# Kernel optimization log

Hardware: AMD Instinct MI355X
Metric: run time of the kernel (lower is better)

## Reference

```python
import jax, jax.numpy as jnp
import numpy as np

I, H, O = 64, 128, 1
H2, H4 = H // 2, H // 4


def _lstm(x, Wih, Whh, bih, bhh, collect_outputs=True):
    # x: [B, T, in]; Wih: [4H, in]; Whh: [4H, H]; gate order i, f, g, o (PyTorch).
    Hh = Whh.shape[1]
    B = x.shape[0]
    # Precompute input contribution for all timesteps: [T, B, 4H]
    xg = (jnp.einsum('bti,gi->btg', x, Wih) + bih + bhh).transpose(1, 0, 2)

    def step(carry, xg_t):
        h, c = carry
        g = xg_t + h @ Whh.T
        i, f, gg, o = jnp.split(g, 4, axis=-1)
        i = jax.nn.sigmoid(i)
        f = jax.nn.sigmoid(f)
        gg = jnp.tanh(gg)
        o = jax.nn.sigmoid(o)
        c = f * c + i * gg
        h = o * jnp.tanh(c)
        return (h, c), (h if collect_outputs else None)

    h0 = jnp.zeros((B, Hh), x.dtype)
    c0 = jnp.zeros((B, Hh), x.dtype)
    (hT, cT), hs = jax.lax.scan(step, (h0, c0), xg)
    if collect_outputs:
        return hs.transpose(1, 0, 2), hT  # [B, T, H], [B, H]
    return None, hT


def setup_inputs() -> dict:
    key = jax.random.key(0)
    ks = jax.random.split(key, 13)
    s1 = 1.0 / np.sqrt(H)
    s2 = 1.0 / np.sqrt(H2)
    s3 = 1.0 / np.sqrt(H4)
    u = lambda k, shape, s: jax.random.uniform(k, shape, jnp.float32, -s, s)
    return {
        'x': jax.random.normal(ks[0], (256, 1024, I), jnp.float32),
        'Wih1': u(ks[1], (4 * H, I), s1),
        'Whh1': u(ks[2], (4 * H, H), s1),
        'bih1': u(ks[3], (4 * H,), s1),
        'bhh1': u(ks[4], (4 * H,), s1),
        'Wih2': u(ks[5], (4 * H2, H), s2),
        'Whh2': u(ks[6], (4 * H2, H2), s2),
        'bih2': u(ks[7], (4 * H2,), s2),
        'bhh2': u(ks[8], (4 * H2,), s2),
        'W1': u(ks[9], (H4, H2), s2),
        'b1': u(ks[10], (H4,), s2),
        'W2': u(ks[11], (O, H4), s3),
        'b2': u(ks[12], (O,), s3),
    }


def reference(x, Wih1, Whh1, bih1, bhh1, Wih2, Whh2, bih2, bhh2, W1, b1, W2, b2):
    out1, _ = _lstm(x, Wih1, Whh1, bih1, bhh1, collect_outputs=True)
    # out[:, -1, :] of layer 2 == its final hidden state
    _, hT = _lstm(out1, Wih2, Whh2, bih2, bhh2, collect_outputs=False)
    h = jax.nn.sigmoid(hT @ W1.T + b1)
    return jax.nn.sigmoid(h @ W2.T + b2)
```

## Files before the change

### kernel.cpp

```cpp
#include <hip/hip_runtime.h>
#include <hip/hip_fp16.h>

#define NB   256
#define TT   1024
#define II   64
#define NT   768

typedef _Float16 f16;
typedef _Float16 f16x4 __attribute__((ext_vector_type(4)));
typedef _Float16 hf8 __attribute__((ext_vector_type(8)));
typedef float    ff4 __attribute__((ext_vector_type(4)));

__device__ __forceinline__ float rcp_fast(float x){
    float r; asm("v_rcp_f32 %0, %1" : "=v"(r) : "v"(x)); return r;
}
__device__ __forceinline__ float exp2_fast(float x){
    float r; asm("v_exp_f32 %0, %1" : "=v"(r) : "v"(x)); return r;
}
__device__ __forceinline__ float sigm(float x){
    return rcp_fast(1.0f + exp2_fast(x * -1.44269504f));
}
__device__ __forceinline__ float tanh_f(float x){
    return fmaf(-2.0f, rcp_fast(1.0f + exp2_fast(x * 2.88539008f)), 1.0f);
}


__launch_bounds__(NT, 3)
__global__ void lstm_mfma(const float* __restrict__ x,
                          const float* __restrict__ Wih1, const float* __restrict__ Whh1,
                          const float* __restrict__ bih1, const float* __restrict__ bhh1,
                          const float* __restrict__ Wih2, const float* __restrict__ Whh2,
                          const float* __restrict__ bih2, const float* __restrict__ bhh2,
                          const float* __restrict__ W1,   const float* __restrict__ b1,
                          const float* __restrict__ W2,   const float* __restrict__ b2,
                          float* __restrict__ out)
{
    __shared__ __align__(16) f16 xchunk[64][II];
    __shared__ __align__(16) f16 h1buf[2][128];
    __shared__ __align__(16) f16 h2buf[2][64];
    __shared__ float headbuf[32];

    const int j    = threadIdx.x;
    const int b    = blockIdx.x;
    const int wave = j >> 6;
    const int lane = j & 63;
    const int rho  = lane & 15;
    const int kg   = lane >> 4;
    const bool l2w = (wave >= 8);

    hf8 A[4][6];
    ff4 bias[4];
    #pragma unroll
    for (int i = 0; i < 4; ++i){
        const int tau = 4*wave + i;
        #pragma unroll
        for (int kt = 0; kt < 6; ++kt){
            const int k = 32*kt + kg*8;
            const float* src;
            if (!l2w){
                const int R = (rho & 3)*128 + 4*tau + (rho >> 2);
                src = (k < 64) ? (Wih1 + R*64 + k) : (Whh1 + R*128 + (k - 64));
            } else {
                const int R = (rho & 3)*64 + 4*(tau - 32) + (rho >> 2);
                src = (k < 128) ? (Wih2 + R*128 + k) : (Whh2 + R*64 + (k - 128));
            }
            float4 v0 = *(const float4*)src;
            float4 v1 = *(const float4*)(src + 4);
            hf8 a;
            a[0]=(f16)v0.x; a[1]=(f16)v0.y; a[2]=(f16)v0.z; a[3]=(f16)v0.w;
            a[4]=(f16)v1.x; a[5]=(f16)v1.y; a[6]=(f16)v1.z; a[7]=(f16)v1.w;
            A[i][kt] = a;
        }
        if (!l2w){
            #pragma unroll
            for (int r = 0; r < 4; ++r){
                const int R = r*128 + 4*tau + kg;
                bias[i][r] = bih1[R] + bhh1[R];
            }
        } else {
            #pragma unroll
            for (int r = 0; r < 4; ++r){
                const int R = r*64 + 4*(tau - 32) + kg;
                bias[i][r] = bih2[R] + bhh2[R];
            }
        }
    }

    const int  sel    = rho >> 2;
    const int  myU    = 4*(4*wave + sel - (l2w ? 32 : 0)) + kg;
    const bool writer = ((lane & 3) == 0);
    float c = 0.0f;

    const float* xb = x + (size_t)b * TT * II;

    if (j < 512){
        float4 v = ((const float4*)xb)[j];
        f16x4 w; w[0]=(f16)v.x; w[1]=(f16)v.y; w[2]=(f16)v.z; w[3]=(f16)v.w;
        *(f16x4*)&xchunk[j >> 4][(j & 15)*4] = w;
    } else if (j < 640){
        h1buf[0][j - 512] = (f16)0.0f;
    } else if (j < 704){
        h2buf[0][j - 640] = (f16)0.0f;
    }
    __syncthreads();

    int cur = 0;
    for (int t = 0; t < TT; ++t){
        const bool do_stage = ((t & 31) == 0) && (t + 32 < TT) && (j < 512);
        float4 sv;
        if (do_stage)
            sv = ((const float4*)(xb + (size_t)(t + 32)*II))[j];

        const f16* xr  = xchunk[t & 63];
        const f16* h1c = h1buf[cur];
        const f16* h2c = h2buf[cur];

        ff4 a0 = bias[0], a1 = bias[1], a2 = bias[2], a3 = bias[3];
        #pragma unroll
        for (int kt = 0; kt < 6; ++kt){
            const f16* bp;
            if (!l2w) bp = (kt < 2) ? (xr  + 32*kt       + kg*8)
                                    : (h1c + 32*(kt - 2) + kg*8);
            else      bp = (kt < 4) ? (h1c + 32*kt       + kg*8)
                                    : (h2c + 32*(kt - 4) + kg*8);
            hf8 bf = *(const hf8*)bp;
            a0 = __builtin_amdgcn_mfma_f32_16x16x32_f16(A[0][kt], bf, a0, 0, 0, 0);
            a1 = __builtin_amdgcn_mfma_f32_16x16x32_f16(A[1][kt], bf, a1, 0, 0, 0);
            a2 = __builtin_amdgcn_mfma_f32_16x16x32_f16(A[2][kt], bf, a2, 0, 0, 0);
            a3 = __builtin_amdgcn_mfma_f32_16x16x32_f16(A[3][kt], bf, a3, 0, 0, 0);
        }

        ff4 a = (sel >= 2) ? ((sel & 1) ? a3 : a2) : ((sel & 1) ? a1 : a0);
        float hv;
        if (l2w && t == 0){
            hv = 0.0f;
        } else {
            float ig = sigm(a[0]);
            float fg = sigm(a[1]);
            float gg = tanh_f(a[2]);
            float og = sigm(a[3]);
            c  = fg*c + ig*gg;
            hv = og * tanh_f(c);
        }
        if (writer){
            if (l2w) h2buf[cur ^ 1][myU] = (f16)hv;
            else     h1buf[cur ^ 1][myU] = (f16)hv;
        }

        if (do_stage){
            f16x4 w; w[0]=(f16)sv.x; w[1]=(f16)sv.y; w[2]=(f16)sv.z; w[3]=(f16)sv.w;
            *(f16x4*)&xchunk[((t + 32) & 63) + (j >> 4)][(j & 15)*4] = w;
        }
        __syncthreads();
        cur ^= 1;
    }

    if (l2w){
        const f16* h1c = h1buf[0];
        const f16* h2c = h2buf[0];
        ff4 a0 = bias[0], a1 = bias[1], a2 = bias[2], a3 = bias[3];
        #pragma unroll
        for (int kt = 0; kt < 6; ++kt){
            const f16* bp = (kt < 4) ? (h1c + 32*kt + kg*8)
                                     : (h2c + 32*(kt - 4) + kg*8);
            hf8 bf = *(const hf8*)bp;
            a0 = __builtin_amdgcn_mfma_f32_16x16x32_f16(A[0][kt], bf, a0, 0, 0, 0);
            a1 = __builtin_amdgcn_mfma_f32_16x16x32_f16(A[1][kt], bf, a1, 0, 0, 0);
            a2 = __builtin_amdgcn_mfma_f32_16x16x32_f16(A[2][kt], bf, a2, 0, 0, 0);
            a3 = __builtin_amdgcn_mfma_f32_16x16x32_f16(A[3][kt], bf, a3, 0, 0, 0);
        }
        ff4 a = (sel >= 2) ? ((sel & 1) ? a3 : a2) : ((sel & 1) ? a1 : a0);
        float ig = sigm(a[0]);
        float fg = sigm(a[1]);
        float gg = tanh_f(a[2]);
        float og = sigm(a[3]);
        c = fg*c + ig*gg;
        float hv = og * tanh_f(c);
        if (writer) h2buf[1][myU] = (f16)hv;
    }
    __syncthreads();

    if (j < 32){
        float a = b1[j];
        const float* w = W1 + j*64;
        #pragma unroll
        for (int k = 0; k < 64; ++k) a = fmaf(w[k], (float)h2buf[1][k], a);
        headbuf[j] = sigm(a);
    }
    __syncthreads();
    if (j == 0){
        float a = b2[0];
        #pragma unroll
        for (int k = 0; k < 32; ++k) a = fmaf(W2[k], headbuf[k], a);
        out[b] = sigm(a);
    }
}

extern "C" void kernel_launch(void* const* d_in, const int* in_sizes, int n_in,
                              void* d_out, int out_size, void* d_ws, size_t ws_size,
                              hipStream_t stream)
{
    (void)in_sizes; (void)n_in; (void)d_ws; (void)ws_size; (void)out_size;
    lstm_mfma<<<NB, NT, 0, stream>>>(
        (const float*)d_in[0],
        (const float*)d_in[1], (const float*)d_in[2],
        (const float*)d_in[3], (const float*)d_in[4],
        (const float*)d_in[5], (const float*)d_in[6],
        (const float*)d_in[7], (const float*)d_in[8],
        (const float*)d_in[9], (const float*)d_in[10],
        (const float*)d_in[11], (const float*)d_in[12],
        (float*)d_out);
}
```

Baseline: 1.014 ms.

## Shrink block to 4 waves, each owning 12 gate tiles of both layers

Reduces the block from 12 waves to 4 waves. Each wave now holds weights for 12 MFMA tiles, so one wave can cover rows from both layer 1 and layer 2, and the final gate tile is picked with a select tree. The aim is to make the per-timestep __syncthreads cheaper and to cut cross-wave barrier cost in this latency-bound recurrence. In exchange, each wave runs three times as many serial MFMAs per step, and register pressure rises sharply with 72 hf8 weight fragments plus 12 accumulators.

```diff
diff --git a/kernel.cpp b/kernel.cpp
--- a/kernel.cpp
+++ b/kernel.cpp
@@ -4,7 +4,7 @@
 #define NB   256
 #define TT   1024
 #define II   64
-#define NT   768
+#define NT   256
 
 typedef _Float16 f16;
 typedef _Float16 f16x4 __attribute__((ext_vector_type(4)));
@@ -25,7 +25,7 @@
 }
 
 
-__launch_bounds__(NT, 3)
+__launch_bounds__(NT, 1)
 __global__ void lstm_mfma(const float* __restrict__ x,
                           const float* __restrict__ Wih1, const float* __restrict__ Whh1,
                           const float* __restrict__ bih1, const float* __restrict__ bhh1,
@@ -46,18 +46,18 @@
     const int lane = j & 63;
     const int rho  = lane & 15;
     const int kg   = lane >> 4;
-    const bool l2w = (wave >= 8);
-
-    hf8 A[4][6];
-    ff4 bias[4];
+
+    hf8 A[12][6];
+    ff4 bias[12];
     #pragma unroll
-    for (int i = 0; i < 4; ++i){
-        const int tau = 4*wave + i;
+    for (int i = 0; i < 12; ++i){
+        const int  tau = 12*wave + i;
+        const bool l2  = (tau >= 32);
         #pragma unroll
         for (int kt = 0; kt < 6; ++kt){
             const int k = 32*kt + kg*8;
             const float* src;
-            if (!l2w){
+            if (!l2){
                 const int R = (rho & 3)*128 + 4*tau + (rho >> 2);
                 src = (k < 64) ? (Wih1 + R*64 + k) : (Whh1 + R*128 + (k - 64));
             } else {
@@ -71,112 +71,183 @@
             a[4]=(f16)v1.x; a[5]=(f16)v1.y; a[6]=(f16)v1.z; a[7]=(f16)v1.w;
             A[i][kt] = a;
         }
-        if (!l2w){
-            #pragma unroll
-            for (int r = 0; r < 4; ++r){
-                const int R = r*128 + 4*tau + kg;
-                bias[i][r] = bih1[R] + bhh1[R];
-            }
-        } else {
-            #pragma unroll
-            for (int r = 0; r < 4; ++r){
-                const int R = r*64 + 4*(tau - 32) + kg;
-                bias[i][r] = bih2[R] + bhh2[R];
-            }
-        }
-    }
-
-    const int  sel    = rho >> 2;
-    const int  myU    = 4*(4*wave + sel - (l2w ? 32 : 0)) + kg;
-    const bool writer = ((lane & 3) == 0);
+        #pragma unroll
+        for (int r = 0; r < 4; ++r){
+            if (!l2){ const int R = r*128 + 4*tau + kg;        bias[i][r] = bih1[R] + bhh1[R]; }
+            else    { const int R = r*64  + 4*(tau - 32) + kg; bias[i][r] = bih2[R] + bhh2[R]; }
+        }
+    }
+
+    const int  myTau = 12*wave + rho;
+    const bool isl2  = (myTau >= 32);
+    const int  myU   = isl2 ? 4*(myTau - 32) + kg : 4*myTau + kg;
     float c = 0.0f;
 
     const float* xb = x + (size_t)b * TT * II;
 
-    if (j < 512){
-        float4 v = ((const float4*)xb)[j];
-        f16x4 w; w[0]=(f16)v.x; w[1]=(f16)v.y; w[2]=(f16)v.z; w[3]=(f16)v.w;
-        *(f16x4*)&xchunk[j >> 4][(j & 15)*4] = w;
-    } else if (j < 640){
-        h1buf[0][j - 512] = (f16)0.0f;
-    } else if (j < 704){
-        h2buf[0][j - 640] = (f16)0.0f;
+    {
+        const float4* sp = (const float4*)xb;
+        float4 v0 = sp[2*j], v1 = sp[2*j + 1];
+        hf8 w;
+        w[0]=(f16)v0.x; w[1]=(f16)v0.y; w[2]=(f16)v0.z; w[3]=(f16)v0.w;
+        w[4]=(f16)v1.x; w[5]=(f16)v1.y; w[6]=(f16)v1.z; w[7]=(f16)v1.w;
+        *(hf8*)&xchunk[j >> 3][(j & 7)*8] = w;
+        if (j < 128) h1buf[0][j] = (f16)0.0f;
+        if (j < 64)  h2buf[0][j] = (f16)0.0f;
     }
     __syncthreads();
 
     int cur = 0;
     for (int t = 0; t < TT; ++t){
-        const bool do_stage = ((t & 31) == 0) && (t + 32 < TT) && (j < 512);
-        float4 sv;
-        if (do_stage)
-            sv = ((const float4*)(xb + (size_t)(t + 32)*II))[j];
+        const bool stage = ((t & 31) == 0) && (t + 32 < TT);
+        float4 sv0, sv1;
+        if (stage){
+            const float4* sp = (const float4*)(xb + (size_t)(t + 32)*II);
+            sv0 = sp[2*j]; sv1 = sp[2*j + 1];
+        }
 
         const f16* xr  = xchunk[t & 63];
         const f16* h1c = h1buf[cur];
         const f16* h2c = h2buf[cur];
 
-        ff4 a0 = bias[0], a1 = bias[1], a2 = bias[2], a3 = bias[3];
-        #pragma unroll
-        for (int kt = 0; kt < 6; ++kt){
-            const f16* bp;
-            if (!l2w) bp = (kt < 2) ? (xr  + 32*kt       + kg*8)
-                                    : (h1c + 32*(kt - 2) + kg*8);
-            else      bp = (kt < 4) ? (h1c + 32*kt       + kg*8)
-                                    : (h2c + 32*(kt - 4) + kg*8);
-            hf8 bf = *(const hf8*)bp;
-            a0 = __builtin_amdgcn_mfma_f32_16x16x32_f16(A[0][kt], bf, a0, 0, 0, 0);
-            a1 = __builtin_amdgcn_mfma_f32_16x16x32_f16(A[1][kt], bf, a1, 0, 0, 0);
-            a2 = __builtin_amdgcn_mfma_f32_16x16x32_f16(A[2][kt], bf, a2, 0, 0, 0);
-            a3 = __builtin_amdgcn_mfma_f32_16x16x32_f16(A[3][kt], bf, a3, 0, 0, 0);
-        }
-
-        ff4 a = (sel >= 2) ? ((sel & 1) ? a3 : a2) : ((sel & 1) ? a1 : a0);
+        hf8 bf[8];
+        if (wave <= 2){
+            bf[0] = *(const hf8*)(xr + kg*8);
+            bf[1] = *(const hf8*)(xr + 32 + kg*8);
+        }
+        bf[2] = *(const hf8*)(h1c       + kg*8);
+        bf[3] = *(const hf8*)(h1c + 32  + kg*8);
+        bf[4] = *(const hf8*)(h1c + 64  + kg*8);
+        bf[5] = *(const hf8*)(h1c + 96  + kg*8);
+        if (wave >= 2){
+            bf[6] = *(const hf8*)(h2c      + kg*8);
+            bf[7] = *(const hf8*)(h2c + 32 + kg*8);
+        }
+
+        ff4 acc[12];
+        #pragma unroll
+        for (int i = 0; i < 12; ++i) acc[i] = bias[i];
+
+        if (wave < 2){
+            #pragma unroll
+            for (int kt = 0; kt < 6; ++kt){
+                hf8 bb = bf[kt];
+                #pragma unroll
+                for (int i = 0; i < 12; ++i)
+                    acc[i] = __builtin_amdgcn_mfma_f32_16x16x32_f16(A[i][kt], bb, acc[i], 0, 0, 0);
+            }
+        } else if (wave == 2){
+            #pragma unroll
+            for (int kt = 0; kt < 6; ++kt){
+                hf8 b1f = bf[kt];
+                #pragma unroll
+                for (int i = 0; i < 8; ++i)
+                    acc[i] = __builtin_amdgcn_mfma_f32_16x16x32_f16(A[i][kt], b1f, acc[i], 0, 0, 0);
+                hf8 b2f = bf[kt + 2];
+                #pragma unroll
+                for (int i = 8; i < 12; ++i)
+                    acc[i] = __builtin_amdgcn_mfma_f32_16x16x32_f16(A[i][kt], b2f, acc[i], 0, 0, 0);
+            }
+        } else {
+            #pragma unroll
+            for (int kt = 0; kt < 6; ++kt){
+                hf8 bb = bf[kt + 2];
+                #pragma unroll
+                for (int i = 0; i < 12; ++i)
+                    acc[i] = __builtin_amdgcn_mfma_f32_16x16x32_f16(A[i][kt], bb, acc[i], 0, 0, 0);
+            }
+        }
+
+        ff4 m0 = (rho & 1) ? acc[1]  : acc[0];
+        ff4 m1 = (rho & 1) ? acc[3]  : acc[2];
+        ff4 m2 = (rho & 1) ? acc[5]  : acc[4];
+        ff4 m3 = (rho & 1) ? acc[7]  : acc[6];
+        ff4 m4 = (rho & 1) ? acc[9]  : acc[8];
+        ff4 m5 = (rho & 1) ? acc[11] : acc[10];
+        ff4 n0 = (rho & 2) ? m1 : m0;
+        ff4 n1 = (rho & 2) ? m3 : m2;
+        ff4 n2 = (rho & 2) ? m5 : m4;
+        ff4 p  = (rho & 4) ? n1 : n0;
+        ff4 qd = (rho & 8) ? n2 : p;
+
         float hv;
-        if (l2w && t == 0){
+        if (isl2 && t == 0){
             hv = 0.0f;
         } else {
-            float ig = sigm(a[0]);
-            float fg = sigm(a[1]);
-            float gg = tanh_f(a[2]);
-            float og = sigm(a[3]);
+            float ig = sigm(qd[0]);
+            float fg = sigm(qd[1]);
+            float gg = tanh_f(qd[2]);
+            float og = sigm(qd[3]);
             c  = fg*c + ig*gg;
             hv = og * tanh_f(c);
         }
-        if (writer){
-            if (l2w) h2buf[cur ^ 1][myU] = (f16)hv;
-            else     h1buf[cur ^ 1][myU] = (f16)hv;
-        }
-
-        if (do_stage){
-            f16x4 w; w[0]=(f16)sv.x; w[1]=(f16)sv.y; w[2]=(f16)sv.z; w[3]=(f16)sv.w;
-            *(f16x4*)&xchunk[((t + 32) & 63) + (j >> 4)][(j & 15)*4] = w;
+        if (rho < 12){
+            if (isl2) h2buf[cur ^ 1][myU] = (f16)hv;
+            else      h1buf[cur ^ 1][myU] = (f16)hv;
+        }
+
+        if (stage){
+            hf8 w;
+            w[0]=(f16)sv0.x; w[1]=(f16)sv0.y; w[2]=(f16)sv0.z; w[3]=(f16)sv0.w;
+            w[4]=(f16)sv1.x; w[5]=(f16)sv1.y; w[6]=(f16)sv1.z; w[7]=(f16)sv1.w;
+            *(hf8*)&xchunk[((t + 32) & 63) + (j >> 3)][(j & 7)*8] = w;
         }
         __syncthreads();
         cur ^= 1;
     }
 
-    if (l2w){
+    if (wave >= 2){
         const f16* h1c = h1buf[0];
         const f16* h2c = h2buf[0];
-        ff4 a0 = bias[0], a1 = bias[1], a2 = bias[2], a3 = bias[3];
-        #pragma unroll
-        for (int kt = 0; kt < 6; ++kt){
-            const f16* bp = (kt < 4) ? (h1c + 32*kt + kg*8)
-                                     : (h2c + 32*(kt - 4) + kg*8);
-            hf8 bf = *(const hf8*)bp;
-            a0 = __builtin_amdgcn_mfma_f32_16x16x32_f16(A[0][kt], bf, a0, 0, 0, 0);
-            a1 = __builtin_amdgcn_mfma_f32_16x16x32_f16(A[1][kt], bf, a1, 0, 0, 0);
-            a2 = __builtin_amdgcn_mfma_f32_16x16x32_f16(A[2][kt], bf, a2, 0, 0, 0);
-            a3 = __builtin_amdgcn_mfma_f32_16x16x32_f16(A[3][kt], bf, a3, 0, 0, 0);
-        }
-        ff4 a = (sel >= 2) ? ((sel & 1) ? a3 : a2) : ((sel & 1) ? a1 : a0);
-        float ig = sigm(a[0]);
-        float fg = sigm(a[1]);
-        float gg = tanh_f(a[2]);
-        float og = sigm(a[3]);
-        c = fg*c + ig*gg;
-        float hv = og * tanh_f(c);
-        if (writer) h2buf[1][myU] = (f16)hv;
+        hf8 ebf[6];
+        ebf[0] = *(const hf8*)(h1c      + kg*8);
+        ebf[1] = *(const hf8*)(h1c + 32 + kg*8);
+        ebf[2] = *(const hf8*)(h1c + 64 + kg*8);
+        ebf[3] = *(const hf8*)(h1c + 96 + kg*8);
+        ebf[4] = *(const hf8*)(h2c      + kg*8);
+        ebf[5] = *(const hf8*)(h2c + 32 + kg*8);
+
+        ff4 acc[12];
+        #pragma unroll
+        for (int i = 0; i < 12; ++i) acc[i] = bias[i];
+        if (wave == 2){
+            #pragma unroll
+            for (int kt = 0; kt < 6; ++kt){
+                hf8 bb = ebf[kt];
+                #pragma unroll
+                for (int i = 8; i < 12; ++i)
+                    acc[i] = __builtin_amdgcn_mfma_f32_16x16x32_f16(A[i][kt], bb, acc[i], 0, 0, 0);
+            }
+        } else {
+            #pragma unroll
+            for (int kt = 0; kt < 6; ++kt){
+                hf8 bb = ebf[kt];
+                #pragma unroll
+                for (int i = 0; i < 12; ++i)
+                    acc[i] = __builtin_amdgcn_mfma_f32_16x16x32_f16(A[i][kt], bb, acc[i], 0, 0, 0);
+            }
+        }
+        ff4 m0 = (rho & 1) ? acc[1]  : acc[0];
+        ff4 m1 = (rho & 1) ? acc[3]  : acc[2];
+        ff4 m2 = (rho & 1) ? acc[5]  : acc[4];
+        ff4 m3 = (rho & 1) ? acc[7]  : acc[6];
+        ff4 m4 = (rho & 1) ? acc[9]  : acc[8];
+        ff4 m5 = (rho & 1) ? acc[11] : acc[10];
+        ff4 n0 = (rho & 2) ? m1 : m0;
+        ff4 n1 = (rho & 2) ? m3 : m2;
+        ff4 n2 = (rho & 2) ? m5 : m4;
+        ff4 p  = (rho & 4) ? n1 : n0;
+        ff4 qd = (rho & 8) ? n2 : p;
+
+        if (rho < 12 && isl2){
+            float ig = sigm(qd[0]);
+            float fg = sigm(qd[1]);
+            float gg = tanh_f(qd[2]);
+            float og = sigm(qd[3]);
+            c = fg*c + ig*gg;
+            float hv = og * tanh_f(c);
+            h2buf[1][myU] = (f16)hv;
+        }
     }
     __syncthreads();
 
```

Result: slower. 1.263 ms (+24.6%).

## Batch layer-1 input projection per 16 steps and shrink block to 8 waves

Applied to the files above, without the earlier changes.

The input projection x·Wih1 is taken off the recurrent critical path. Every 16 timesteps all waves compute it for a block of 16 steps with MFMA and store the results in a swizzled shared-memory buffer, and the per-step MFMA for layer 1 then only covers the Whh1 term. The block drops from 12 to 8 waves, so each layer-1 wave now handles 8 tiles with 4 k-steps instead of 4 tiles with 6. This means fewer waves take part in each per-step barrier, and x is prefetched into registers ahead of use. In exchange, register pressure rises (32 A fragments plus AX per thread), an extra barrier is added every 16 steps, and the selection of gate outputs gets more complex.

```diff
diff --git a/kernel.cpp b/kernel.cpp
--- a/kernel.cpp
+++ b/kernel.cpp
@@ -4,10 +4,9 @@
 #define NB   256
 #define TT   1024
 #define II   64
-#define NT   768
+#define NT   512
 
 typedef _Float16 f16;
-typedef _Float16 f16x4 __attribute__((ext_vector_type(4)));
 typedef _Float16 hf8 __attribute__((ext_vector_type(8)));
 typedef float    ff4 __attribute__((ext_vector_type(4)));
 
@@ -23,9 +22,20 @@
 __device__ __forceinline__ float tanh_f(float x){
     return fmaf(-2.0f, rcp_fast(1.0f + exp2_fast(x * 2.88539008f)), 1.0f);
 }
-
-
-__launch_bounds__(NT, 3)
+__device__ __forceinline__ hf8 cvt8(float4 a, float4 b){
+    hf8 r;
+    r[0]=(f16)a.x; r[1]=(f16)a.y; r[2]=(f16)a.z; r[3]=(f16)a.w;
+    r[4]=(f16)b.x; r[5]=(f16)b.y; r[6]=(f16)b.z; r[7]=(f16)b.w;
+    return r;
+}
+__device__ __forceinline__ hf8 ldw8(const float* src){
+    float4 v0 = *(const float4*)src;
+    float4 v1 = *(const float4*)(src + 4);
+    return cvt8(v0, v1);
+}
+
+
+__launch_bounds__(NT, 2)
 __global__ void lstm_mfma(const float* __restrict__ x,
                           const float* __restrict__ Wih1, const float* __restrict__ Whh1,
                           const float* __restrict__ bih1, const float* __restrict__ bhh1,
@@ -35,7 +45,7 @@
                           const float* __restrict__ W2,   const float* __restrict__ b2,
                           float* __restrict__ out)
 {
-    __shared__ __align__(16) f16 xchunk[64][II];
+    __shared__ __align__(16) float xg[16][128][4];
     __shared__ __align__(16) f16 h1buf[2][128];
     __shared__ __align__(16) f16 h2buf[2][64];
     __shared__ float headbuf[32];
@@ -46,110 +56,181 @@
     const int lane = j & 63;
     const int rho  = lane & 15;
     const int kg   = lane >> 4;
-    const bool l2w = (wave >= 8);
-
-    hf8 A[4][6];
-    ff4 bias[4];
+    const bool l2w = (wave >= 4);
+
+    const float* xb = x + (size_t)b * TT * II;
+
+    float4 xl0, xl1, xl2, xl3;
+    {
+        const float* xp = xb + (size_t)rho * II + kg*8;
+        xl0 = *(const float4*)xp;
+        xl1 = *(const float4*)(xp + 4);
+        xl2 = *(const float4*)(xp + 32);
+        xl3 = *(const float4*)(xp + 36);
+    }
+
+    hf8 A[32];
+    if (!l2w){
+        #pragma unroll
+        for (int i = 0; i < 8; ++i){
+            const int tau = 8*wave + i;
+            const int R   = (rho & 3)*128 + 4*tau + (rho >> 2);
+            #pragma unroll
+            for (int kt = 0; kt < 4; ++kt)
+                A[i*4 + kt] = ldw8(Whh1 + R*128 + 32*kt + kg*8);
+        }
+    } else {
+        #pragma unroll
+        for (int i = 0; i < 4; ++i){
+            const int tau2 = 4*(wave - 4) + i;
+            const int R    = (rho & 3)*64 + 4*tau2 + (rho >> 2);
+            #pragma unroll
+            for (int kt = 0; kt < 6; ++kt)
+                A[i*6 + kt] = ldw8((kt < 4) ? (Wih2 + R*128 + 32*kt + kg*8)
+                                            : (Whh2 + R*64  + 32*(kt-4) + kg*8));
+        }
+    }
+    hf8 AX[8];
+    ff4 biasX[4];
     #pragma unroll
     for (int i = 0; i < 4; ++i){
         const int tau = 4*wave + i;
-        #pragma unroll
-        for (int kt = 0; kt < 6; ++kt){
-            const int k = 32*kt + kg*8;
-            const float* src;
-            if (!l2w){
-                const int R = (rho & 3)*128 + 4*tau + (rho >> 2);
-                src = (k < 64) ? (Wih1 + R*64 + k) : (Whh1 + R*128 + (k - 64));
-            } else {
-                const int R = (rho & 3)*64 + 4*(tau - 32) + (rho >> 2);
-                src = (k < 128) ? (Wih2 + R*128 + k) : (Whh2 + R*64 + (k - 128));
-            }
-            float4 v0 = *(const float4*)src;
-            float4 v1 = *(const float4*)(src + 4);
-            hf8 a;
-            a[0]=(f16)v0.x; a[1]=(f16)v0.y; a[2]=(f16)v0.z; a[3]=(f16)v0.w;
-            a[4]=(f16)v1.x; a[5]=(f16)v1.y; a[6]=(f16)v1.z; a[7]=(f16)v1.w;
-            A[i][kt] = a;
-        }
-        if (!l2w){
+        const int R   = (rho & 3)*128 + 4*tau + (rho >> 2);
+        #pragma unroll
+        for (int kkt = 0; kkt < 2; ++kkt)
+            AX[i*2 + kkt] = ldw8(Wih1 + R*64 + 32*kkt + kg*8);
+        #pragma unroll
+        for (int r = 0; r < 4; ++r){
+            const int Rb = r*128 + 4*tau + kg;
+            biasX[i][r] = bih1[Rb] + bhh1[Rb];
+        }
+    }
+    ff4 bias2[4];
+    if (l2w){
+        #pragma unroll
+        for (int i = 0; i < 4; ++i)
             #pragma unroll
             for (int r = 0; r < 4; ++r){
-                const int R = r*128 + 4*tau + kg;
-                bias[i][r] = bih1[R] + bhh1[R];
-            }
-        } else {
-            #pragma unroll
-            for (int r = 0; r < 4; ++r){
-                const int R = r*64 + 4*(tau - 32) + kg;
-                bias[i][r] = bih2[R] + bhh2[R];
-            }
-        }
-    }
-
-    const int  sel    = rho >> 2;
-    const int  myU    = 4*(4*wave + sel - (l2w ? 32 : 0)) + kg;
-    const bool writer = ((lane & 3) == 0);
+                const int Rb = r*64 + 4*(4*(wave-4) + i) + kg;
+                bias2[i][r] = bih2[Rb] + bhh2[Rb];
+            }
+    }
+
+    if (j < 128) h1buf[0][j] = (f16)0.0f;
+    if (j < 64)  h2buf[0][j] = (f16)0.0f;
+
+    {
+        hf8 xh0 = cvt8(xl0, xl1);
+        hf8 xh1 = cvt8(xl2, xl3);
+        ff4 g0 = biasX[0], g1 = biasX[1], g2 = biasX[2], g3 = biasX[3];
+        g0 = __builtin_amdgcn_mfma_f32_16x16x32_f16(AX[0], xh0, g0, 0, 0, 0);
+        g1 = __builtin_amdgcn_mfma_f32_16x16x32_f16(AX[2], xh0, g1, 0, 0, 0);
+        g2 = __builtin_amdgcn_mfma_f32_16x16x32_f16(AX[4], xh0, g2, 0, 0, 0);
+        g3 = __builtin_amdgcn_mfma_f32_16x16x32_f16(AX[6], xh0, g3, 0, 0, 0);
+        g0 = __builtin_amdgcn_mfma_f32_16x16x32_f16(AX[1], xh1, g0, 0, 0, 0);
+        g1 = __builtin_amdgcn_mfma_f32_16x16x32_f16(AX[3], xh1, g1, 0, 0, 0);
+        g2 = __builtin_amdgcn_mfma_f32_16x16x32_f16(AX[5], xh1, g2, 0, 0, 0);
+        g3 = __builtin_amdgcn_mfma_f32_16x16x32_f16(AX[7], xh1, g3, 0, 0, 0);
+        const int sw = rho & 7;
+        *(ff4*)&xg[rho][(4*(4*wave+0)+kg) ^ sw][0] = g0;
+        *(ff4*)&xg[rho][(4*(4*wave+1)+kg) ^ sw][0] = g1;
+        *(ff4*)&xg[rho][(4*(4*wave+2)+kg) ^ sw][0] = g2;
+        *(ff4*)&xg[rho][(4*(4*wave+3)+kg) ^ sw][0] = g3;
+    }
+    __syncthreads();
+
     float c = 0.0f;
-
-    const float* xb = x + (size_t)b * TT * II;
-
-    if (j < 512){
-        float4 v = ((const float4*)xb)[j];
-        f16x4 w; w[0]=(f16)v.x; w[1]=(f16)v.y; w[2]=(f16)v.z; w[3]=(f16)v.w;
-        *(f16x4*)&xchunk[j >> 4][(j & 15)*4] = w;
-    } else if (j < 640){
-        h1buf[0][j - 512] = (f16)0.0f;
-    } else if (j < 704){
-        h2buf[0][j - 640] = (f16)0.0f;
-    }
-    __syncthreads();
-
     int cur = 0;
     for (int t = 0; t < TT; ++t){
-        const bool do_stage = ((t & 31) == 0) && (t + 32 < TT) && (j < 512);
-        float4 sv;
-        if (do_stage)
-            sv = ((const float4*)(xb + (size_t)(t + 32)*II))[j];
-
-        const f16* xr  = xchunk[t & 63];
+        const int trow = t & 15;
+
+        if (trow == 14 && t + 2 < TT){
+            const float* xp = xb + (size_t)(t + 2 + rho) * II + kg*8;
+            xl0 = *(const float4*)xp;
+            xl1 = *(const float4*)(xp + 4);
+            xl2 = *(const float4*)(xp + 32);
+            xl3 = *(const float4*)(xp + 36);
+        }
+
         const f16* h1c = h1buf[cur];
         const f16* h2c = h2buf[cur];
-
-        ff4 a0 = bias[0], a1 = bias[1], a2 = bias[2], a3 = bias[3];
-        #pragma unroll
-        for (int kt = 0; kt < 6; ++kt){
-            const f16* bp;
-            if (!l2w) bp = (kt < 2) ? (xr  + 32*kt       + kg*8)
-                                    : (h1c + 32*(kt - 2) + kg*8);
-            else      bp = (kt < 4) ? (h1c + 32*kt       + kg*8)
-                                    : (h2c + 32*(kt - 4) + kg*8);
-            hf8 bf = *(const hf8*)bp;
-            a0 = __builtin_amdgcn_mfma_f32_16x16x32_f16(A[0][kt], bf, a0, 0, 0, 0);
-            a1 = __builtin_amdgcn_mfma_f32_16x16x32_f16(A[1][kt], bf, a1, 0, 0, 0);
-            a2 = __builtin_amdgcn_mfma_f32_16x16x32_f16(A[2][kt], bf, a2, 0, 0, 0);
-            a3 = __builtin_amdgcn_mfma_f32_16x16x32_f16(A[3][kt], bf, a3, 0, 0, 0);
-        }
-
-        ff4 a = (sel >= 2) ? ((sel & 1) ? a3 : a2) : ((sel & 1) ? a1 : a0);
-        float hv;
-        if (l2w && t == 0){
-            hv = 0.0f;
+        const int  sx  = trow & 7;
+
+        hf8 bf0 = *(const hf8*)(h1c      + kg*8);
+        hf8 bf1 = *(const hf8*)(h1c + 32 + kg*8);
+        hf8 bf2 = *(const hf8*)(h1c + 64 + kg*8);
+        hf8 bf3 = *(const hf8*)(h1c + 96 + kg*8);
+
+        if (!l2w){
+            ff4 acc[8];
+            #pragma unroll
+            for (int i = 0; i < 8; ++i)
+                acc[i] = *(const ff4*)&xg[trow][(4*(8*wave+i)+kg) ^ sx][0];
+            #pragma unroll
+            for (int kt = 0; kt < 4; ++kt){
+                hf8 bb = (kt==0)?bf0:(kt==1)?bf1:(kt==2)?bf2:bf3;
+                #pragma unroll
+                for (int i = 0; i < 8; ++i)
+                    acc[i] = __builtin_amdgcn_mfma_f32_16x16x32_f16(A[i*4+kt], bb, acc[i], 0, 0, 0);
+            }
+            ff4 m0 = (rho & 1) ? acc[1] : acc[0];
+            ff4 m1 = (rho & 1) ? acc[3] : acc[2];
+            ff4 m2 = (rho & 1) ? acc[5] : acc[4];
+            ff4 m3 = (rho & 1) ? acc[7] : acc[6];
+            ff4 n0 = (rho & 2) ? m1 : m0;
+            ff4 n1 = (rho & 2) ? m3 : m2;
+            ff4 qd = (rho & 4) ? n1 : n0;
+            float ig = sigm(qd[0]), fg = sigm(qd[1]);
+            float gg = tanh_f(qd[2]), og = sigm(qd[3]);
+            c = fg*c + ig*gg;
+            float hv = og * tanh_f(c);
+            if (rho < 8) h1buf[cur ^ 1][4*(8*wave + rho) + kg] = (f16)hv;
         } else {
-            float ig = sigm(a[0]);
-            float fg = sigm(a[1]);
-            float gg = tanh_f(a[2]);
-            float og = sigm(a[3]);
-            c  = fg*c + ig*gg;
-            hv = og * tanh_f(c);
-        }
-        if (writer){
-            if (l2w) h2buf[cur ^ 1][myU] = (f16)hv;
-            else     h1buf[cur ^ 1][myU] = (f16)hv;
-        }
-
-        if (do_stage){
-            f16x4 w; w[0]=(f16)sv.x; w[1]=(f16)sv.y; w[2]=(f16)sv.z; w[3]=(f16)sv.w;
-            *(f16x4*)&xchunk[((t + 32) & 63) + (j >> 4)][(j & 15)*4] = w;
+            hf8 bf4 = *(const hf8*)(h2c      + kg*8);
+            hf8 bf5 = *(const hf8*)(h2c + 32 + kg*8);
+            ff4 acc[4];
+            #pragma unroll
+            for (int i = 0; i < 4; ++i) acc[i] = bias2[i];
+            #pragma unroll
+            for (int kt = 0; kt < 6; ++kt){
+                hf8 bb = (kt==0)?bf0:(kt==1)?bf1:(kt==2)?bf2:(kt==3)?bf3:(kt==4)?bf4:bf5;
+                #pragma unroll
+                for (int i = 0; i < 4; ++i)
+                    acc[i] = __builtin_amdgcn_mfma_f32_16x16x32_f16(A[i*6+kt], bb, acc[i], 0, 0, 0);
+            }
+            ff4 m0 = (rho & 1) ? acc[1] : acc[0];
+            ff4 m1 = (rho & 1) ? acc[3] : acc[2];
+            ff4 qd = (rho & 2) ? m1 : m0;
+            float hv;
+            if (t > 0){
+                float ig = sigm(qd[0]), fg = sigm(qd[1]);
+                float gg = tanh_f(qd[2]), og = sigm(qd[3]);
+                c = fg*c + ig*gg;
+                hv = og * tanh_f(c);
+            } else {
+                hv = 0.0f;
+            }
+            if (rho < 4) h2buf[cur ^ 1][4*(4*(wave-4) + rho) + kg] = (f16)hv;
+        }
+
+        if (trow == 15 && t + 1 < TT){
+            __syncthreads();
+            hf8 xh0 = cvt8(xl0, xl1);
+            hf8 xh1 = cvt8(xl2, xl3);
+            ff4 g0 = biasX[0], g1 = biasX[1], g2 = biasX[2], g3 = biasX[3];
+            g0 = __builtin_amdgcn_mfma_f32_16x16x32_f16(AX[0], xh0, g0, 0, 0, 0);
+            g1 = __builtin_amdgcn_mfma_f32_16x16x32_f16(AX[2], xh0, g1, 0, 0, 0);
+            g2 = __builtin_amdgcn_mfma_f32_16x16x32_f16(AX[4], xh0, g2, 0, 0, 0);
+            g3 = __builtin_amdgcn_mfma_f32_16x16x32_f16(AX[6], xh0, g3, 0, 0, 0);
+            g0 = __builtin_amdgcn_mfma_f32_16x16x32_f16(AX[1], xh1, g0, 0, 0, 0);
+            g1 = __builtin_amdgcn_mfma_f32_16x16x32_f16(AX[3], xh1, g1, 0, 0, 0);
+            g2 = __builtin_amdgcn_mfma_f32_16x16x32_f16(AX[5], xh1, g2, 0, 0, 0);
+            g3 = __builtin_amdgcn_mfma_f32_16x16x32_f16(AX[7], xh1, g3, 0, 0, 0);
+            const int sw = rho & 7;
+            *(ff4*)&xg[rho][(4*(4*wave+0)+kg) ^ sw][0] = g0;
+            *(ff4*)&xg[rho][(4*(4*wave+1)+kg) ^ sw][0] = g1;
+            *(ff4*)&xg[rho][(4*(4*wave+2)+kg) ^ sw][0] = g2;
+            *(ff4*)&xg[rho][(4*(4*wave+3)+kg) ^ sw][0] = g3;
         }
         __syncthreads();
         cur ^= 1;
@@ -158,25 +239,30 @@
     if (l2w){
         const f16* h1c = h1buf[0];
         const f16* h2c = h2buf[0];
-        ff4 a0 = bias[0], a1 = bias[1], a2 = bias[2], a3 = bias[3];
+        hf8 bf0 = *(const hf8*)(h1c      + kg*8);
+        hf8 bf1 = *(const hf8*)(h1c + 32 + kg*8);
+        hf8 bf2 = *(const hf8*)(h1c + 64 + kg*8);
+        hf8 bf3 = *(const hf8*)(h1c + 96 + kg*8);
+        hf8 bf4 = *(const hf8*)(h2c      + kg*8);
+        hf8 bf5 = *(const hf8*)(h2c + 32 + kg*8);
+        ff4 acc[4];
+        #pragma unroll
+        for (int i = 0; i < 4; ++i) acc[i] = bias2[i];
         #pragma unroll
         for (int kt = 0; kt < 6; ++kt){
-            const f16* bp = (kt < 4) ? (h1c + 32*kt + kg*8)
-                                     : (h2c + 32*(kt - 4) + kg*8);
-            hf8 bf = *(const hf8*)bp;
-            a0 = __builtin_amdgcn_mfma_f32_16x16x32_f16(A[0][kt], bf, a0, 0, 0, 0);
-            a1 = __builtin_amdgcn_mfma_f32_16x16x32_f16(A[1][kt], bf, a1, 0, 0, 0);
-            a2 = __builtin_amdgcn_mfma_f32_16x16x32_f16(A[2][kt], bf, a2, 0, 0, 0);
-            a3 = __builtin_amdgcn_mfma_f32_16x16x32_f16(A[3][kt], bf, a3, 0, 0, 0);
-        }
-        ff4 a = (sel >= 2) ? ((sel & 1) ? a3 : a2) : ((sel & 1) ? a1 : a0);
-        float ig = sigm(a[0]);
-        float fg = sigm(a[1]);
-        float gg = tanh_f(a[2]);
-        float og = sigm(a[3]);
+            hf8 bb = (kt==0)?bf0:(kt==1)?bf1:(kt==2)?bf2:(kt==3)?bf3:(kt==4)?bf4:bf5;
+            #pragma unroll
+            for (int i = 0; i < 4; ++i)
+                acc[i] = __builtin_amdgcn_mfma_f32_16x16x32_f16(A[i*6+kt], bb, acc[i], 0, 0, 0);
+        }
+        ff4 m0 = (rho & 1) ? acc[1] : acc[0];
+        ff4 m1 = (rho & 1) ? acc[3] : acc[2];
+        ff4 qd = (rho & 2) ? m1 : m0;
+        float ig = sigm(qd[0]), fg = sigm(qd[1]);
+        float gg = tanh_f(qd[2]), og = sigm(qd[3]);
         c = fg*c + ig*gg;
         float hv = og * tanh_f(c);
-        if (writer) h2buf[1][myU] = (f16)hv;
+        if (rho < 4) h2buf[1][4*(4*(wave-4) + rho) + kg] = (f16)hv;
     }
     __syncthreads();
 
```

New measurement: 1.062 ms. +4.7%, slower.
